# Kernel tuning notes

Measured on AMD Instinct MI355X. Metric: run time of the kernel, lower is better.

The kernel has to match this reference:

```python
import jax, jax.numpy as jnp
import numpy as np

N_GRAPHS = 512


def setup_inputs() -> dict:
    key = jax.random.key(0)
    ks = jax.random.split(key, 9)
    N, E, V, NE, D, C = 100000, 500000, 50000, 1000000, 300, 20
    nodes_batch = jax.random.randint(ks[0], (N,), 0, V)
    edges_batch = jax.random.randint(ks[1], (E,), 0, NE)
    src = jax.random.randint(ks[2], (E,), 0, N)
    dst = jax.random.randint(ks[3], (E,), 0, N)
    graph_ids = jnp.sort(jax.random.randint(ks[4], (N,), 0, N_GRAPHS))
    node_embed = jax.random.normal(ks[5], (V, D), dtype=jnp.float32)
    edge_embed = jax.random.uniform(ks[6], (NE, 1), dtype=jnp.float32)
    fc_w = jax.random.normal(ks[7], (D, C), dtype=jnp.float32) * 0.05
    fc_b = jnp.zeros((C,), dtype=jnp.float32)
    return {"nodes_batch": nodes_batch, "edges_batch": edges_batch, "src": src,
            "dst": dst, "graph_ids": graph_ids, "node_embed": node_embed,
            "edge_embed": edge_embed, "fc_w": fc_w, "fc_b": fc_b}


def reference(nodes_batch, edges_batch, src, dst, graph_ids, node_embed, edge_embed, fc_w, fc_b):
    N = nodes_batch.shape[0]
    h = node_embed[nodes_batch]                      # [N, D] node features
    w = edge_embed[edges_batch]                      # [E, 1] scalar edge weights
    msg = h[src] * w                                 # [E, D] src_mul_edge
    # DGL mean reduce over incoming edges; nodes with no in-edges get 0.
    summed = jax.ops.segment_sum(msg, dst, num_segments=N)
    cnt = jax.ops.segment_sum(jnp.ones((msg.shape[0],), msg.dtype), dst, num_segments=N)
    h_new = summed / jnp.maximum(cnt, 1.0)[:, None]  # [N, D]
    g = jax.ops.segment_sum(h_new, graph_ids, num_segments=N_GRAPHS)  # sum_nodes readout
    out = jax.nn.relu(g) @ fc_w + fc_b               # dropout is identity at eval
    return out
```

## Files before the change

### kernel.cpp

```cpp
#include <hip/hip_runtime.h>
#include <hip/hip_bf16.h>

#define NG 512
#define D_DIM 300
#define C_DIM 20
#define NSLICE 8
#define NBINS (NSLICE * NG)
#define GSTRIDE 304
#define SC_EPB 2048

static __device__ inline ushort f2bf(float f) {
    union { float f; unsigned u; } x; x.f = f;
    unsigned r = x.u + 0x7FFF + ((x.u >> 16) & 1);
    return (ushort)(r >> 16);
}

__global__ __launch_bounds__(256) void convert_b(const float* __restrict__ B,
                                                 ushort* __restrict__ B16, int K) {
    int total = K * 38;
    for (int idx = blockIdx.x * 256 + threadIdx.x; idx < total; idx += gridDim.x * 256) {
        int row = idx / 38;
        int k = idx - row * 38;
        int d0 = k * 8;
        const float* p = B + (size_t)row * D_DIM + d0;
        float f0, f1, f2, f3, f4, f5, f6, f7;
        if (d0 + 8 <= D_DIM) {
            float4 a = *(const float4*)p;
            float4 b = *(const float4*)(p + 4);
            f0 = a.x; f1 = a.y; f2 = a.z; f3 = a.w;
            f4 = b.x; f5 = b.y; f6 = b.z; f7 = b.w;
        } else {
            float4 a = *(const float4*)p;
            f0 = a.x; f1 = a.y; f2 = a.z; f3 = a.w;
            f4 = f5 = f6 = f7 = 0.f;
        }
        uint4 pk;
        pk.x = (unsigned)f2bf(f0) | ((unsigned)f2bf(f1) << 16);
        pk.y = (unsigned)f2bf(f2) | ((unsigned)f2bf(f3) << 16);
        pk.z = (unsigned)f2bf(f4) | ((unsigned)f2bf(f5) << 16);
        pk.w = (unsigned)f2bf(f6) | ((unsigned)f2bf(f7) << 16);
        *(uint4*)(B16 + (size_t)row * GSTRIDE + d0) = pk;
    }
}

__global__ __launch_bounds__(1024) void count_hist(const int* __restrict__ dst,
                                                   const int* __restrict__ src,
                                                   const int* __restrict__ nodes_batch,
                                                   const int* __restrict__ graph_ids,
                                                   int* __restrict__ cnt,
                                                   int* __restrict__ kcnt,
                                                   int E, int KS) {
    __shared__ int h[NBINS];
    int t = threadIdx.x;
    for (int i = t; i < NBINS; i += 1024) h[i] = 0;
    __syncthreads();
    for (int e = blockIdx.x * 1024 + t; e < E; e += gridDim.x * 1024) {
        int d = dst[e];
        atomicAdd(&cnt[d], 1);
        int v = nodes_batch[src[e]];
        int g = graph_ids[d];
        atomicAdd(&h[(v / KS) * NG + g], 1);
    }
    __syncthreads();
    for (int i = t; i < NBINS; i += 1024)
        if (h[i]) atomicAdd(&kcnt[i], h[i]);
}

__global__ __launch_bounds__(1024) void scan4k(const int* __restrict__ kcnt,
                                               int* __restrict__ koff,
                                               int* __restrict__ kfill, int E) {
    __shared__ int s[1024];
    int t = threadIdx.x;
    int l0 = kcnt[t * 4 + 0], l1 = kcnt[t * 4 + 1], l2 = kcnt[t * 4 + 2], l3 = kcnt[t * 4 + 3];
    int sum = l0 + l1 + l2 + l3;
    s[t] = sum;
    __syncthreads();
    for (int off = 1; off < 1024; off <<= 1) {
        int x = (t >= off) ? s[t - off] : 0;
        __syncthreads();
        s[t] += x;
        __syncthreads();
    }
    int base = s[t] - sum;
    int v0 = base, v1 = base + l0, v2 = base + l0 + l1, v3 = base + l0 + l1 + l2;
    koff[t * 4 + 0] = v0; kfill[t * 4 + 0] = v0;
    koff[t * 4 + 1] = v1; kfill[t * 4 + 1] = v1;
    koff[t * 4 + 2] = v2; kfill[t * 4 + 2] = v2;
    koff[t * 4 + 3] = v3; kfill[t * 4 + 3] = v3;
    if (t == 1023) koff[NBINS] = E;
}

__global__ __launch_bounds__(512) void scatter4k(const int* __restrict__ src,
                                                 const int* __restrict__ dst,
                                                 const int* __restrict__ eb,
                                                 const int* __restrict__ nodes_batch,
                                                 const float* __restrict__ edge_embed,
                                                 const int* __restrict__ graph_ids,
                                                 const int* __restrict__ cnt,
                                                 int* __restrict__ kfill,
                                                 int2* __restrict__ elist, int E, int KS) {
    __shared__ int bcnt[NBINS];
    __shared__ int base[NBINS];
    int t = threadIdx.x;
    int e0 = blockIdx.x * SC_EPB;
    for (int i = t; i < NBINS; i += 512) bcnt[i] = 0;
    __syncthreads();
    int vs[SC_EPB / 512];
    float scales[SC_EPB / 512];
    int keys[SC_EPB / 512];
#pragma unroll
    for (int k = 0; k < SC_EPB / 512; k++) {
        int e = e0 + k * 512 + t;
        keys[k] = -1;
        if (e < E) {
            int d = dst[e];
            int v = nodes_batch[src[e]];
            keys[k] = (v / KS) * NG + graph_ids[d];
            vs[k] = v;
            scales[k] = edge_embed[eb[e]] / (float)max(cnt[d], 1);
            atomicAdd(&bcnt[keys[k]], 1);
        }
    }
    __syncthreads();
    for (int i = t; i < NBINS; i += 512) {
        int c = bcnt[i];
        base[i] = c ? atomicAdd(&kfill[i], c) : 0;
        bcnt[i] = 0;
    }
    __syncthreads();
#pragma unroll
    for (int k = 0; k < SC_EPB / 512; k++) {
        if (keys[k] >= 0) {
            int pos = base[keys[k]] + atomicAdd(&bcnt[keys[k]], 1);
            elist[pos] = make_int2(vs[k], __float_as_int(scales[k]));
        }
    }
}

static __device__ inline void acc8(uint4 q, float s, float* a) {
    a[0] += s * __uint_as_float(q.x << 16);
    a[1] += s * __uint_as_float(q.x & 0xFFFF0000u);
    a[2] += s * __uint_as_float(q.y << 16);
    a[3] += s * __uint_as_float(q.y & 0xFFFF0000u);
    a[4] += s * __uint_as_float(q.z << 16);
    a[5] += s * __uint_as_float(q.z & 0xFFFF0000u);
    a[6] += s * __uint_as_float(q.w << 16);
    a[7] += s * __uint_as_float(q.w & 0xFFFF0000u);
}

__global__ __launch_bounds__(256, 4) void accum_wave(const int2* __restrict__ elist,
                                                     const int* __restrict__ koff,
                                                     const ushort* __restrict__ B16,
                                                     float* __restrict__ gslice) {
    int t = threadIdx.x;
    int wv = t >> 6, lane = t & 63;
    if (lane >= 38) return;
    int slice = blockIdx.x & 7;
    int g = ((blockIdx.x >> 3) << 2) + wv;
    int bin = slice * NG + g;
    int beg = koff[bin], end = koff[bin + 1];
    const ushort* Bl = B16 + (lane << 3);

    float a[8] = {0.f, 0.f, 0.f, 0.f, 0.f, 0.f, 0.f, 0.f};
    int j = beg;
    for (; j + 8 <= end; j += 8) {
        int2 p0 = elist[j + 0], p1 = elist[j + 1], p2 = elist[j + 2], p3 = elist[j + 3];
        int2 p4 = elist[j + 4], p5 = elist[j + 5], p6 = elist[j + 6], p7 = elist[j + 7];
        uint4 q0 = *(const uint4*)(Bl + (size_t)p0.x * GSTRIDE);
        uint4 q1 = *(const uint4*)(Bl + (size_t)p1.x * GSTRIDE);
        uint4 q2 = *(const uint4*)(Bl + (size_t)p2.x * GSTRIDE);
        uint4 q3 = *(const uint4*)(Bl + (size_t)p3.x * GSTRIDE);
        uint4 q4 = *(const uint4*)(Bl + (size_t)p4.x * GSTRIDE);
        uint4 q5 = *(const uint4*)(Bl + (size_t)p5.x * GSTRIDE);
        uint4 q6 = *(const uint4*)(Bl + (size_t)p6.x * GSTRIDE);
        uint4 q7 = *(const uint4*)(Bl + (size_t)p7.x * GSTRIDE);
        acc8(q0, __int_as_float(p0.y), a);
        acc8(q1, __int_as_float(p1.y), a);
        acc8(q2, __int_as_float(p2.y), a);
        acc8(q3, __int_as_float(p3.y), a);
        acc8(q4, __int_as_float(p4.y), a);
        acc8(q5, __int_as_float(p5.y), a);
        acc8(q6, __int_as_float(p6.y), a);
        acc8(q7, __int_as_float(p7.y), a);
    }
    for (; j + 4 <= end; j += 4) {
        int2 p0 = elist[j + 0], p1 = elist[j + 1], p2 = elist[j + 2], p3 = elist[j + 3];
        uint4 q0 = *(const uint4*)(Bl + (size_t)p0.x * GSTRIDE);
        uint4 q1 = *(const uint4*)(Bl + (size_t)p1.x * GSTRIDE);
        uint4 q2 = *(const uint4*)(Bl + (size_t)p2.x * GSTRIDE);
        uint4 q3 = *(const uint4*)(Bl + (size_t)p3.x * GSTRIDE);
        acc8(q0, __int_as_float(p0.y), a);
        acc8(q1, __int_as_float(p1.y), a);
        acc8(q2, __int_as_float(p2.y), a);
        acc8(q3, __int_as_float(p3.y), a);
    }
    for (; j < end; ++j) {
        int2 pr = elist[j];
        uint4 q = *(const uint4*)(Bl + (size_t)pr.x * GSTRIDE);
        acc8(q, __int_as_float(pr.y), a);
    }
    float4* outp = (float4*)(gslice + (size_t)bin * GSTRIDE + (lane << 3));
    outp[0] = make_float4(a[0], a[1], a[2], a[3]);
    outp[1] = make_float4(a[4], a[5], a[6], a[7]);
}

__global__ __launch_bounds__(320) void fc_kernel(const float* __restrict__ gslice,
                                                 const float* __restrict__ fc_w,
                                                 const float* __restrict__ fc_b,
                                                 float* __restrict__ out) {
    __shared__ float wlds[D_DIM * C_DIM];
    __shared__ float accs[D_DIM];
    __shared__ float outs[C_DIM];
    int gid = blockIdx.x;
    int t = threadIdx.x;
    for (int i = t; i < D_DIM * C_DIM; i += 320) wlds[i] = fc_w[i];
    if (t < D_DIM) {
        float a = 0.f;
#pragma unroll
        for (int s = 0; s < NSLICE; s++)
            a += gslice[(size_t)(s * NG + gid) * GSTRIDE + t];
        accs[t] = a;
    }
    if (t < C_DIM) outs[t] = fc_b[t];
    __syncthreads();
    if (t < C_DIM * 12) {
        int c = t % C_DIM;
        int ch = t / C_DIM;
        float p = 0.f;
#pragma unroll
        for (int d = ch * 25; d < ch * 25 + 25; d++) {
            float gv = accs[d];
            gv = gv > 0.f ? gv : 0.f;
            p += gv * wlds[d * C_DIM + c];
        }
        atomicAdd(&outs[c], p);
    }
    __syncthreads();
    if (t < C_DIM) out[gid * C_DIM + t] = outs[t];
}

extern "C" void kernel_launch(void* const* d_in, const int* in_sizes, int n_in,
                              void* d_out, int out_size, void* d_ws, size_t ws_size,
                              hipStream_t stream) {
    const int* nodes_batch = (const int*)d_in[0];
    const int* edges_batch = (const int*)d_in[1];
    const int* src = (const int*)d_in[2];
    const int* dst = (const int*)d_in[3];
    const int* graph_ids = (const int*)d_in[4];
    const float* node_embed = (const float*)d_in[5];
    const float* edge_embed = (const float*)d_in[6];
    const float* fc_w = (const float*)d_in[7];
    const float* fc_b = (const float*)d_in[8];
    float* out = (float*)d_out;

    int N = in_sizes[0];
    int E = in_sizes[2];
    int K = in_sizes[5] / D_DIM;
    int KS = (K + NSLICE - 1) / NSLICE;

    char* ws = (char*)d_ws;
    size_t off = 0;
    int* cnt = (int*)(ws + off); off += (size_t)N * 4;
    int* kcnt = (int*)(ws + off); off += (size_t)NBINS * 4;
    int* koff = (int*)(ws + off); off += (size_t)(NBINS + 1) * 4;
    int* kfill = (int*)(ws + off); off += (size_t)NBINS * 4;
    off = (off + 15) & ~(size_t)15;
    ushort* B16 = (ushort*)(ws + off); off += (size_t)K * GSTRIDE * 2;
    float* gslice = (float*)(ws + off); off += (size_t)NBINS * GSTRIDE * 4;
    int2* elist = (int2*)(ws + off); off += (size_t)E * 8;

    if (ws_size >= off) {
        hipMemsetAsync(cnt, 0, (size_t)N * 4, stream);
        hipMemsetAsync(kcnt, 0, (size_t)NBINS * 4, stream);
        convert_b<<<2048, 256, 0, stream>>>(node_embed, B16, K);
        count_hist<<<256, 1024, 0, stream>>>(dst, src, nodes_batch, graph_ids, cnt, kcnt, E, KS);
        scan4k<<<1, 1024, 0, stream>>>(kcnt, koff, kfill, E);
        int nsb = (E + SC_EPB - 1) / SC_EPB;
        scatter4k<<<nsb, 512, 0, stream>>>(src, dst, edges_batch, nodes_batch, edge_embed,
                                           graph_ids, cnt, kfill, elist, E, KS);
        accum_wave<<<8 * (NG / 4), 256, 0, stream>>>(elist, koff, B16, gslice);
        fc_kernel<<<NG, 320, 0, stream>>>(gslice, fc_w, fc_b, out);
    }
}
```

Baseline: 117.5 us.

## Precompute packed edge keys in histogram pass and split accumulation bins across waves

The histogram kernel now computes each edge's bin, node id and edge weight once and stores them packed into a temporary int2 array, so the scatter kernel no longer repeats the dependent gathers through src, nodes_batch, graph_ids and edge_embed. The accumulation kernel gives each bin to two waves, one per half of its edge range, doubling the grid and writing two partial slices that the FC kernel sums. The scatter block size is halved and the bf16 conversion loop handles two elements per iteration. The cost is an extra 4 MB array write and read, plus twice the partial-slice storage and reads.

```diff
diff --git a/kernel.cpp b/kernel.cpp
--- a/kernel.cpp
+++ b/kernel.cpp
@@ -7,7 +7,7 @@
 #define NSLICE 8
 #define NBINS (NSLICE * NG)
 #define GSTRIDE 304
-#define SC_EPB 2048
+#define SC_EPB 1024
 
 static __device__ inline ushort f2bf(float f) {
     union { float f; unsigned u; } x; x.f = f;
@@ -18,37 +18,46 @@
 __global__ __launch_bounds__(256) void convert_b(const float* __restrict__ B,
                                                  ushort* __restrict__ B16, int K) {
     int total = K * 38;
-    for (int idx = blockIdx.x * 256 + threadIdx.x; idx < total; idx += gridDim.x * 256) {
-        int row = idx / 38;
-        int k = idx - row * 38;
-        int d0 = k * 8;
-        const float* p = B + (size_t)row * D_DIM + d0;
-        float f0, f1, f2, f3, f4, f5, f6, f7;
-        if (d0 + 8 <= D_DIM) {
-            float4 a = *(const float4*)p;
-            float4 b = *(const float4*)(p + 4);
-            f0 = a.x; f1 = a.y; f2 = a.z; f3 = a.w;
-            f4 = b.x; f5 = b.y; f6 = b.z; f7 = b.w;
-        } else {
-            float4 a = *(const float4*)p;
-            f0 = a.x; f1 = a.y; f2 = a.z; f3 = a.w;
-            f4 = f5 = f6 = f7 = 0.f;
-        }
-        uint4 pk;
-        pk.x = (unsigned)f2bf(f0) | ((unsigned)f2bf(f1) << 16);
-        pk.y = (unsigned)f2bf(f2) | ((unsigned)f2bf(f3) << 16);
-        pk.z = (unsigned)f2bf(f4) | ((unsigned)f2bf(f5) << 16);
-        pk.w = (unsigned)f2bf(f6) | ((unsigned)f2bf(f7) << 16);
-        *(uint4*)(B16 + (size_t)row * GSTRIDE + d0) = pk;
+    int gs = gridDim.x * 256;
+    for (int i0 = blockIdx.x * 256 + threadIdx.x; i0 < total; i0 += 2 * gs) {
+        int i1 = i0 + gs;
+        bool ok1 = i1 < total;
+        int r0 = i0 / 38, k0 = i0 - r0 * 38, d00 = k0 * 8;
+        int r1, k1, d01 = 0;
+        if (ok1) { r1 = i1 / 38; k1 = i1 - r1 * 38; d01 = k1 * 8; }
+        const float* p0 = B + (size_t)r0 * D_DIM + d00;
+        const float* p1 = ok1 ? (B + (size_t)r1 * D_DIM + d01) : p0;
+        float4 a0 = *(const float4*)p0;
+        float4 b0 = (d00 + 8 <= D_DIM) ? *(const float4*)(p0 + 4) : make_float4(0.f, 0.f, 0.f, 0.f);
+        float4 a1 = *(const float4*)p1;
+        float4 b1 = (d01 + 8 <= D_DIM) ? *(const float4*)(p1 + 4) : make_float4(0.f, 0.f, 0.f, 0.f);
+        if (d00 + 8 > D_DIM) {  }
+        uint4 q0;
+        q0.x = (unsigned)f2bf(a0.x) | ((unsigned)f2bf(a0.y) << 16);
+        q0.y = (unsigned)f2bf(a0.z) | ((unsigned)f2bf(a0.w) << 16);
+        q0.z = (unsigned)f2bf(b0.x) | ((unsigned)f2bf(b0.y) << 16);
+        q0.w = (unsigned)f2bf(b0.z) | ((unsigned)f2bf(b0.w) << 16);
+        *(uint4*)(B16 + (size_t)r0 * GSTRIDE + d00) = q0;
+        if (ok1) {
+            uint4 q1;
+            q1.x = (unsigned)f2bf(a1.x) | ((unsigned)f2bf(a1.y) << 16);
+            q1.y = (unsigned)f2bf(a1.z) | ((unsigned)f2bf(a1.w) << 16);
+            q1.z = (unsigned)f2bf(b1.x) | ((unsigned)f2bf(b1.y) << 16);
+            q1.w = (unsigned)f2bf(b1.z) | ((unsigned)f2bf(b1.w) << 16);
+            *(uint4*)(B16 + (size_t)r1 * GSTRIDE + d01) = q1;
+        }
     }
 }
 
 __global__ __launch_bounds__(1024) void count_hist(const int* __restrict__ dst,
                                                    const int* __restrict__ src,
+                                                   const int* __restrict__ eb,
                                                    const int* __restrict__ nodes_batch,
                                                    const int* __restrict__ graph_ids,
+                                                   const float* __restrict__ edge_embed,
                                                    int* __restrict__ cnt,
                                                    int* __restrict__ kcnt,
+                                                   int2* __restrict__ pkey2,
                                                    int E, int KS) {
     __shared__ int h[NBINS];
     int t = threadIdx.x;
@@ -57,9 +66,12 @@
     for (int e = blockIdx.x * 1024 + t; e < E; e += gridDim.x * 1024) {
         int d = dst[e];
         atomicAdd(&cnt[d], 1);
-        int v = nodes_batch[src[e]];
+        unsigned v = (unsigned)nodes_batch[src[e]];
         int g = graph_ids[d];
-        atomicAdd(&h[(v / KS) * NG + g], 1);
+        int bin = (int)(v / (unsigned)KS) * NG + g;
+        float w = edge_embed[eb[e]];
+        pkey2[e] = make_int2((int)((v << 12) | (unsigned)bin), __float_as_int(w));
+        atomicAdd(&h[bin], 1);
     }
     __syncthreads();
     for (int i = t; i < NBINS; i += 1024)
@@ -90,15 +102,11 @@
     if (t == 1023) koff[NBINS] = E;
 }
 
-__global__ __launch_bounds__(512) void scatter4k(const int* __restrict__ src,
+__global__ __launch_bounds__(512) void scatter4k(const int2* __restrict__ pkey2,
                                                  const int* __restrict__ dst,
-                                                 const int* __restrict__ eb,
-                                                 const int* __restrict__ nodes_batch,
-                                                 const float* __restrict__ edge_embed,
-                                                 const int* __restrict__ graph_ids,
                                                  const int* __restrict__ cnt,
                                                  int* __restrict__ kfill,
-                                                 int2* __restrict__ elist, int E, int KS) {
+                                                 int2* __restrict__ elist, int E) {
     __shared__ int bcnt[NBINS];
     __shared__ int base[NBINS];
     int t = threadIdx.x;
@@ -113,11 +121,12 @@
         int e = e0 + k * 512 + t;
         keys[k] = -1;
         if (e < E) {
+            int2 pk = pkey2[e];
+            unsigned u = (unsigned)pk.x;
+            keys[k] = (int)(u & 4095u);
+            vs[k] = (int)(u >> 12);
             int d = dst[e];
-            int v = nodes_batch[src[e]];
-            keys[k] = (v / KS) * NG + graph_ids[d];
-            vs[k] = v;
-            scales[k] = edge_embed[eb[e]] / (float)max(cnt[d], 1);
+            scales[k] = __int_as_float(pk.y) / (float)max(cnt[d], 1);
             atomicAdd(&bcnt[keys[k]], 1);
         }
     }
@@ -156,9 +165,13 @@
     int wv = t >> 6, lane = t & 63;
     if (lane >= 38) return;
     int slice = blockIdx.x & 7;
-    int g = ((blockIdx.x >> 3) << 2) + wv;
+    int g = ((blockIdx.x >> 3) << 1) + (wv >> 1);
+    int h = wv & 1;
     int bin = slice * NG + g;
-    int beg = koff[bin], end = koff[bin + 1];
+    int b0 = koff[bin], b1 = koff[bin + 1];
+    int mid = (b0 + b1) >> 1;
+    int beg = h ? mid : b0;
+    int end = h ? b1 : mid;
     const ushort* Bl = B16 + (lane << 3);
 
     float a[8] = {0.f, 0.f, 0.f, 0.f, 0.f, 0.f, 0.f, 0.f};
@@ -199,7 +212,7 @@
         uint4 q = *(const uint4*)(Bl + (size_t)pr.x * GSTRIDE);
         acc8(q, __int_as_float(pr.y), a);
     }
-    float4* outp = (float4*)(gslice + (size_t)bin * GSTRIDE + (lane << 3));
+    float4* outp = (float4*)(gslice + (size_t)(h * NBINS + bin) * GSTRIDE + (lane << 3));
     outp[0] = make_float4(a[0], a[1], a[2], a[3]);
     outp[1] = make_float4(a[4], a[5], a[6], a[7]);
 }
@@ -217,8 +230,8 @@
     if (t < D_DIM) {
         float a = 0.f;
 #pragma unroll
-        for (int s = 0; s < NSLICE; s++)
-            a += gslice[(size_t)(s * NG + gid) * GSTRIDE + t];
+        for (int p = 0; p < 2 * NSLICE; p++)
+            a += gslice[(size_t)(p * NG + gid) * GSTRIDE + t];
         accs[t] = a;
     }
     if (t < C_DIM) outs[t] = fc_b[t];
@@ -266,19 +279,20 @@
     int* kfill = (int*)(ws + off); off += (size_t)NBINS * 4;
     off = (off + 15) & ~(size_t)15;
     ushort* B16 = (ushort*)(ws + off); off += (size_t)K * GSTRIDE * 2;
-    float* gslice = (float*)(ws + off); off += (size_t)NBINS * GSTRIDE * 4;
+    float* gslice = (float*)(ws + off); off += (size_t)2 * NBINS * GSTRIDE * 4;
+    int2* pkey2 = (int2*)(ws + off); off += (size_t)E * 8;
     int2* elist = (int2*)(ws + off); off += (size_t)E * 8;
 
     if (ws_size >= off) {
         hipMemsetAsync(cnt, 0, (size_t)N * 4, stream);
         hipMemsetAsync(kcnt, 0, (size_t)NBINS * 4, stream);
         convert_b<<<2048, 256, 0, stream>>>(node_embed, B16, K);
-        count_hist<<<256, 1024, 0, stream>>>(dst, src, nodes_batch, graph_ids, cnt, kcnt, E, KS);
+        count_hist<<<256, 1024, 0, stream>>>(dst, src, edges_batch, nodes_batch, graph_ids,
+                                             edge_embed, cnt, kcnt, pkey2, E, KS);
         scan4k<<<1, 1024, 0, stream>>>(kcnt, koff, kfill, E);
         int nsb = (E + SC_EPB - 1) / SC_EPB;
-        scatter4k<<<nsb, 512, 0, stream>>>(src, dst, edges_batch, nodes_batch, edge_embed,
-                                           graph_ids, cnt, kfill, elist, E, KS);
-        accum_wave<<<8 * (NG / 4), 256, 0, stream>>>(elist, koff, B16, gslice);
+        scatter4k<<<nsb, 512, 0, stream>>>(pkey2, dst, cnt, kfill, elist, E);
+        accum_wave<<<8 * (NG / 2), 256, 0, stream>>>(elist, koff, B16, gslice);
         fc_kernel<<<NG, 320, 0, stream>>>(gslice, fc_w, fc_b, out);
     }
 }
```

New measurement: 123.0 us. 4.6% more time.
